# Kernel optimization log

Measured on AMD Instinct MI355X. Metric: run time of the kernel, lower is better.

Reference implementation:

```python
import jax, jax.numpy as jnp
import numpy as np

NUM_GROUPS = 32
EPS = 1e-6


def group_norm(x, gamma, beta):
    # x: [B, C, H, W]; GroupNorm over (channels-in-group, H, W)
    B, C, H, W = x.shape
    xg = x.reshape(B, NUM_GROUPS, C // NUM_GROUPS, H, W)
    mean = xg.mean(axis=(2, 3, 4), keepdims=True)
    var = xg.var(axis=(2, 3, 4), keepdims=True)
    xn = ((xg - mean) * jax.lax.rsqrt(var + EPS)).reshape(B, C, H, W)
    return xn * gamma[None, :, None, None] + beta[None, :, None, None]


def conv1x1(x, w, b):
    # 1x1 conv == channel-mixing matmul. w: [C_out, C_in]
    return jnp.einsum('bchw,oc->bohw', x, w) + b[None, :, None, None]


def setup_inputs() -> dict:
    key = jax.random.key(0)
    ks = jax.random.split(key, 6)
    B, C, H, W = 8, 256, 64, 64
    s = 1.0 / np.sqrt(C)  # fan-in scaled weights (like Conv2d default)
    inp = {
        'x': jax.random.normal(ks[0], (B, C, H, W), jnp.float32),
        'gamma': jnp.ones((C,), jnp.float32),
        'beta': jnp.zeros((C,), jnp.float32),
        'wq': jax.random.normal(ks[1], (C, C), jnp.float32) * s,
        'bq': jnp.zeros((C,), jnp.float32),
        'wk': jax.random.normal(ks[2], (C, C), jnp.float32) * s,
        'bk': jnp.zeros((C,), jnp.float32),
        'wv': jax.random.normal(ks[3], (C, C), jnp.float32) * s,
        'bv': jnp.zeros((C,), jnp.float32),
        'wo': jax.random.normal(ks[4], (C, C), jnp.float32) * s,
        'bo': jnp.zeros((C,), jnp.float32),
    }
    return inp


def reference(x, gamma, beta, wq, bq, wk, bk, wv, bv, wo, bo):
    B, C, H, W = x.shape
    h = group_norm(x, gamma, beta)
    q = conv1x1(h, wq, bq)
    k = conv1x1(h, wk, bk)
    v = conv1x1(h, wv, bv)
    # elu + 1 feature map (nonnegative kernel features)
    q = jax.nn.elu(q) + 1.0
    k = jax.nn.elu(k) + 1.0
    N = H * W
    kf = k.reshape(B, C, N)            # [B, C, N]
    vf = v.reshape(B, C, N)            # [B, C, N]
    qf = q.reshape(B, C, N)            # [B, C, N]
    # kv = k @ v^T : [B, C, C]
    kv = jnp.einsum('bcn,bdn->bcd', kf, vf)
    # h_out[b, n, d] = sum_c q[b, c, n] * kv[b, c, d]; stored channel-first
    h_out = jnp.einsum('bcn,bcd->bdn', qf, kv).reshape(B, C, H, W)
    return x + conv1x1(h_out, wo, bo)
```

## Files before the change

### kernel.cpp

```cpp
#include <hip/hip_runtime.h>
#include <math.h>

#define C_DIM 256
#define N_DIM 4096
#define B_DIM 8

typedef __attribute__((ext_vector_type(8))) short bf16x8;
typedef __attribute__((ext_vector_type(4))) float f32x4;
typedef __attribute__((ext_vector_type(8))) unsigned short us8;
typedef __attribute__((ext_vector_type(4))) unsigned short us4;

__device__ inline unsigned short f2bf(float f) {
    unsigned int u = __float_as_uint(f);
    u += 0x7fffu + ((u >> 16) & 1u);
    return (unsigned short)(u >> 16);
}

__device__ inline void gload_lds16(const void* g, void* l) {
    __builtin_amdgcn_global_load_lds(
        (const __attribute__((address_space(1))) unsigned int*)g,
        (__attribute__((address_space(3))) unsigned int*)l, 16, 0, 0);
}

__global__ __launch_bounds__(256) void prep_kernel(
    const float* __restrict__ wq, const float* __restrict__ wk,
    const float* __restrict__ wv, const float* __restrict__ wo,
    const float* __restrict__ bk, const float* __restrict__ bv,
    const float* __restrict__ x,
    unsigned short* __restrict__ wqb, unsigned short* __restrict__ wkvb,
    unsigned short* __restrict__ wob, float* __restrict__ bkv,
    float2* __restrict__ sums)
{
    int z = blockIdx.x;
    int t = threadIdx.x;
    if (z < 256) {
        const float* s; unsigned short* d;
        int which = z >> 6;
        if (which == 0)      { s = wq; d = wqb; }
        else if (which == 1) { s = wk; d = wkvb; }
        else if (which == 2) { s = wv; d = wkvb + 65536; }
        else                 { s = wo; d = wob; }
        int idx = (z & 63) * 1024 + t * 4;
        float4 v = *(const float4*)(s + idx);
        us4 r; r[0] = f2bf(v.x); r[1] = f2bf(v.y); r[2] = f2bf(v.z); r[3] = f2bf(v.w);
        *(us4*)(d + idx) = r;
    } else if (z == 256) {
        bkv[t]       = bk[t];
        bkv[t + 256] = bv[t];
    } else {
        int bc = z - 257;
        const float* xc = x + (size_t)bc * N_DIM;
        float s = 0.f, q = 0.f;
        for (int i = t; i < 1024; i += 256) {
            float4 v = ((const float4*)xc)[i];
            s += v.x + v.y + v.z + v.w;
            q += v.x*v.x + v.y*v.y + v.z*v.z + v.w*v.w;
        }
        #pragma unroll
        for (int off = 32; off > 0; off >>= 1) {
            s += __shfl_down(s, off);
            q += __shfl_down(q, off);
        }
        __shared__ float red[8];
        int w = t >> 6;
        if ((t & 63) == 0) { red[w*2] = s; red[w*2+1] = q; }
        __syncthreads();
        if (t == 0) {
            sums[bc] = make_float2(red[0]+red[2]+red[4]+red[6],
                                   red[1]+red[3]+red[5]+red[7]);
        }
    }
}

__global__ __launch_bounds__(256) void gn_apply(const float* __restrict__ x,
                                                const float2* __restrict__ sums,
                                                const float* __restrict__ gamma,
                                                const float* __restrict__ beta,
                                                unsigned short* __restrict__ hT) {
    int b = blockIdx.y, n0 = blockIdx.x * 64;
    int t = threadIdx.x;
    __shared__ float scale[256], shift[256];
    __shared__ unsigned short trans[64][264];

    {
        int c = t;
        int gbase = c & ~7;
        float s = 0.f, q = 0.f;
        #pragma unroll
        for (int j = 0; j < 8; j++) {
            float2 u = sums[b*256 + gbase + j];
            s += u.x; q += u.y;
        }
        float mean = s * (1.f/32768.f);
        float var  = q * (1.f/32768.f) - mean*mean;
        float inv  = rsqrtf(var + 1e-6f);
        float gm = gamma[c] * inv;
        scale[c] = gm;
        shift[c] = beta[c] - mean * gm;
    }
    __syncthreads();

    #pragma unroll
    for (int it = 0; it < 16; it++) {
        int c  = it*16 + (t >> 4);
        int nl = (t & 15) * 4;
        float4 v = *(const float4*)(x + ((size_t)(b*C_DIM + c))*N_DIM + n0 + nl);
        float sc = scale[c], sh = shift[c];
        trans[nl+0][c] = f2bf(v.x*sc + sh);
        trans[nl+1][c] = f2bf(v.y*sc + sh);
        trans[nl+2][c] = f2bf(v.z*sc + sh);
        trans[nl+3][c] = f2bf(v.w*sc + sh);
    }
    __syncthreads();

    #pragma unroll
    for (int it = 0; it < 8; it++) {
        int nl = it*8 + (t >> 5);
        int cb = (t & 31) * 8;
        us8 vv = *(us8*)&trans[nl][cb];
        *(us8*)(hT + ((size_t)b*N_DIM + n0 + nl)*C_DIM + cb) = vv;
    }
}

__global__ __launch_bounds__(256) void kvred(const float* __restrict__ src, unsigned short* __restrict__ dst) {
    int gi = (blockIdx.x * 256 + threadIdx.x) * 4;
    int b = gi >> 16, idx = gi & 65535;
    float4 a = make_float4(0.f,0.f,0.f,0.f);
    #pragma unroll
    for (int sp = 0; sp < 8; sp++) {
        float4 v = *(const float4*)(src + (((size_t)b*8 + sp) << 16) + idx);
        a.x += v.x; a.y += v.y; a.z += v.z; a.w += v.w;
    }
    us4 r; r[0] = f2bf(a.x); r[1] = f2bf(a.y); r[2] = f2bf(a.z); r[3] = f2bf(a.w);
    *(us4*)(dst + ((size_t)b << 16) + idx) = r;
}

template<int RI, int RJ, int MODE>
__device__ __forceinline__ void gemm2_body(
    const unsigned short* __restrict__ Ab,
    const unsigned short* __restrict__ Bb,
    const float* __restrict__ bias,
    unsigned short* __restrict__ Cp,
    int crow0, int ccol0, bool elu, char* smem)
{
    constexpr int M = RI * 32, N = RJ * 32;
    constexpr int ACH = M / 64;
    constexpr int BCH = N / 64;
    unsigned short* lds = (unsigned short*)smem;

    int t = threadIdx.x;
    int w = t >> 6, l = t & 63;
    int wm = w >> 1, wn = w & 1;
    int l15 = l & 15, quad = l >> 4;

    f32x4 acc[RI][RJ];
    #pragma unroll
    for (int i = 0; i < RI; i++)
        #pragma unroll
        for (int j = 0; j < RJ; j++)
            #pragma unroll
            for (int r = 0; r < 4; r++) acc[i][j][r] = 0.f;

    auto stage = [&](int buf, int kt) {
        unsigned short* Ls = lds + buf * (M*32 + N*32);
        #pragma unroll
        for (int s = 0; s < ACH; s++) {
            int c = t + s*256, row = c >> 2;
            int cs = (c & 3) ^ ((row >> 1) & 3);
            gload_lds16(Ab + (size_t)row*256 + kt + cs*8, Ls + c*8);
        }
        #pragma unroll
        for (int s = 0; s < BCH; s++) {
            int c = t + s*256, row = c >> 2;
            int cs = (c & 3) ^ ((row >> 1) & 3);
            gload_lds16(Bb + (size_t)row*256 + kt + cs*8, Ls + M*32 + c*8);
        }
    };

    stage(0, 0);
    stage(1, 32);

    int acol = (quad ^ ((l15 >> 1) & 3)) * 8;

    int bufc = 0;
    for (int kt = 0; kt < 8; ++kt) {
        if (kt + 1 < 8) asm volatile("s_waitcnt vmcnt(6)" ::: "memory");
        else            asm volatile("s_waitcnt vmcnt(0)" ::: "memory");
        __builtin_amdgcn_s_barrier();
        __builtin_amdgcn_sched_barrier(0);
        if (kt + 2 < 8) {
            int bufn = bufc + 2; if (bufn >= 3) bufn -= 3;
            stage(bufn, (kt + 2) * 32);
        }
        __builtin_amdgcn_sched_barrier(0);

        const unsigned short* As = lds + bufc * (M*32 + N*32);
        const unsigned short* Bs = As + M*32;
        bf16x8 af[RI], bfr[RJ];
        #pragma unroll
        for (int i = 0; i < RI; i++)
            af[i]  = *(const bf16x8*)(As + (wm*(RI*16) + i*16 + l15)*32 + acol);
        #pragma unroll
        for (int j = 0; j < RJ; j++)
            bfr[j] = *(const bf16x8*)(Bs + (wn*(RJ*16) + j*16 + l15)*32 + acol);
        __builtin_amdgcn_s_setprio(1);
        #pragma unroll
        for (int i = 0; i < RI; i++)
            #pragma unroll
            for (int j = 0; j < RJ; j++)
                acc[i][j] = __builtin_amdgcn_mfma_f32_16x16x32_bf16(af[i], bfr[j], acc[i][j], 0, 0, 0);
        __builtin_amdgcn_s_setprio(0);
        bufc = (bufc == 2) ? 0 : bufc + 1;
    }
    __syncthreads();

    if (MODE == 0) {
        unsigned short* ep = (unsigned short*)smem;
        #pragma unroll
        for (int h = 0; h < 2; h++) {
            if (wm == h) {
                #pragma unroll
                for (int i = 0; i < RI; i++) {
                    #pragma unroll
                    for (int j = 0; j < RJ; j++) {
                        int cl = wn*128 + j*16 + l15;
                        float bi = bias[cl];
                        #pragma unroll
                        for (int r = 0; r < 4; r++) {
                            int rl = quad*4 + i*16 + r;
                            float val = acc[i][j][r] + bi;
                            val = val > 0.f ? val + 1.f : __expf(val);
                            ep[rl*264 + cl] = f2bf(val);
                        }
                    }
                }
            }
            __syncthreads();
            #pragma unroll
            for (int it = 0; it < 8; it++) {
                int row = it*8 + (t >> 5);
                int colc = (t & 31) * 8;
                us8 vv = *(us8*)(ep + row*264 + colc);
                *(us8*)(Cp + (size_t)(crow0 + h*64 + row)*256 + colc) = vv;
            }
            __syncthreads();
        }
    } else {
        unsigned short* ep = (unsigned short*)smem;
        #pragma unroll
        for (int h = 0; h < 2; h++) {
            if (wm == h) {
                #pragma unroll
                for (int i = 0; i < RI; i++) {
                    #pragma unroll
                    for (int j = 0; j < RJ; j++) {
                        int cl = wn*64 + j*16 + l15;
                        #pragma unroll
                        for (int r = 0; r < 4; r++) {
                            int rl = quad*4 + i*16 + r;
                            float val = acc[i][j][r] + bias[crow0 + h*128 + rl];
                            if (elu) val = val > 0.f ? val + 1.f : __expf(val);
                            ep[rl*136 + cl] = f2bf(val);
                        }
                    }
                }
            }
            __syncthreads();
            #pragma unroll
            for (int it = 0; it < 8; it++) {
                int row = it*16 + (t >> 4);
                int colc = (t & 15) * 8;
                us8 vv = *(us8*)(ep + row*136 + colc);
                *(us8*)(Cp + (size_t)(crow0 + h*128 + row)*4096 + ccol0 + colc) = vv;
            }
            __syncthreads();
        }
    }
}

__global__ __launch_bounds__(256, 2) void qkv2(
    const unsigned short* __restrict__ hT, const unsigned short* __restrict__ wqb,
    const unsigned short* __restrict__ wkvb,
    const float* __restrict__ bq, const float* __restrict__ bkv,
    unsigned short* __restrict__ qT, unsigned short* __restrict__ kvbuf)
{
    __shared__ __align__(16) char smem[73728];
    int z = blockIdx.x;
    if (z < 256) {
        int b = z >> 5, m_blk = (z & 31) * 128;
        gemm2_body<4,8,0>(hT + (size_t)b*1048576 + (size_t)m_blk*256, wqb,
                          bq, qT + (size_t)b*1048576, m_blk, 0, true, smem);
    } else {
        int iz = z - 256;
        int b = iz >> 6, rem = iz & 63;
        int mh = rem >> 5, n_blk = (rem & 31) * 128;
        gemm2_body<8,4,1>(wkvb + (size_t)mh*65536,
                          hT + (size_t)b*1048576 + (size_t)n_blk*256,
                          bkv, kvbuf + (size_t)b*2097152,
                          mh*256, n_blk, mh == 0, smem);
    }
}

template<int MODE>
__device__ __forceinline__ void gemm_body(
    const unsigned short* __restrict__ Ab, const unsigned short* __restrict__ Bb,
    const float* __restrict__ bias, const float* __restrict__ residb,
    void* __restrict__ Cb,
    int N, int K, int k0, int Ks, int m_blk, int n_blk, char* smem)
{
    unsigned short* lds = (unsigned short*)smem;

    int t = threadIdx.x;
    int w = t >> 6, l = t & 63;
    int wm = w >> 1, wn = w & 1;
    int l15 = l & 15, quad = l >> 4;

    int srow = w * 16 + (l >> 2);
    int skc  = (((l & 3) ^ ((l >> 3) & 3)) * 8);

    f32x4 acc[4][4];
    #pragma unroll
    for (int i = 0; i < 4; i++)
        #pragma unroll
        for (int j = 0; j < 4; j++)
            #pragma unroll
            for (int r = 0; r < 4; r++) acc[i][j][r] = 0.f;

    auto stage = [&](int buf, int kt) {
        unsigned short* Asl = lds + buf*8192 + t*8;
        unsigned short* Bsl = Asl + 4096;
        #pragma unroll
        for (int rep = 0; rep < 2; rep++) {
            gload_lds16(Ab + (size_t)(m_blk + rep*64 + srow) * K + kt + skc, Asl + rep*2048);
            gload_lds16(Bb + (size_t)(n_blk + rep*64 + srow) * K + kt + skc, Bsl + rep*2048);
        }
    };

    const int nt = Ks >> 5;

    stage(0, k0);
    if (nt > 1) stage(1, k0 + 32);

    int acol = (quad ^ ((l15 >> 1) & 3)) * 8;

    int bufc = 0;
    for (int kt = 0; kt < nt; ++kt) {
        if (kt + 1 < nt) asm volatile("s_waitcnt vmcnt(4)" ::: "memory");
        else             asm volatile("s_waitcnt vmcnt(0)" ::: "memory");
        __builtin_amdgcn_s_barrier();
        __builtin_amdgcn_sched_barrier(0);
        if (kt + 2 < nt) {
            int bufn = bufc + 2; if (bufn >= 3) bufn -= 3;
            stage(bufn, k0 + (kt + 2) * 32);
        }
        __builtin_amdgcn_sched_barrier(0);

        const unsigned short* Aw = lds + bufc*8192 + (wm*64 + l15)*32 + acol;
        const unsigned short* Bw = lds + bufc*8192 + 4096 + (wn*64 + l15)*32 + acol;
        bf16x8 af[4], bfr[4];
        #pragma unroll
        for (int i = 0; i < 4; i++) af[i]  = *(const bf16x8*)(Aw + i*512);
        #pragma unroll
        for (int j = 0; j < 4; j++) bfr[j] = *(const bf16x8*)(Bw + j*512);
        __builtin_amdgcn_s_setprio(1);
        #pragma unroll
        for (int i = 0; i < 4; i++)
            #pragma unroll
            for (int j = 0; j < 4; j++)
                acc[i][j] = __builtin_amdgcn_mfma_f32_16x16x32_bf16(af[i], bfr[j], acc[i][j], 0, 0, 0);
        __builtin_amdgcn_s_setprio(0);
        bufc = (bufc == 2) ? 0 : bufc + 1;
    }
    __syncthreads();

    if (MODE == 4) {
        unsigned short* ep = (unsigned short*)smem;
        unsigned short* Cp = (unsigned short*)Cb;
        #pragma unroll
        for (int h = 0; h < 2; h++) {
            if (wm == h) {
                int row0 = quad*4;
                int col0 = wn*64 + l15;
                #pragma unroll
                for (int i = 0; i < 4; i++)
                    #pragma unroll
                    for (int j = 0; j < 4; j++)
                        #pragma unroll
                        for (int r = 0; r < 4; r++)
                            ep[(row0 + i*16 + r)*136 + col0 + j*16] = f2bf(acc[i][j][r]);
            }
            __syncthreads();
            #pragma unroll
            for (int it = 0; it < 4; it++) {
                int row = it*16 + (t >> 4);
                int col = (t & 15) * 8;
                us8 vv = *(us8*)(ep + row*136 + col);
                *(us8*)(Cp + (size_t)(m_blk + h*64 + row) * N + n_blk + col) = vv;
            }
            __syncthreads();
        }
    } else {
        float* ep32 = (float*)smem;
        float* Cp = (float*)Cb;
        #pragma unroll
        for (int h = 0; h < 2; h++) {
            if (wm == h) {
                int row0 = quad*4;
                int col0 = wn*64 + l15;
                #pragma unroll
                for (int i = 0; i < 4; i++)
                    #pragma unroll
                    for (int j = 0; j < 4; j++)
                        #pragma unroll
                        for (int r = 0; r < 4; r++)
                            ep32[(row0 + i*16 + r)*140 + col0 + j*16] = acc[i][j][r];
            }
            __syncthreads();
            #pragma unroll
            for (int it = 0; it < 8; it++) {
                int rl  = it*8 + (t >> 5);
                int row = m_blk + h*64 + rl;
                int col = (t & 31) * 4;
                f32x4 vv = *(f32x4*)(ep32 + rl*140 + col);
                if (MODE == 5) {
                    float bi = bias[row];
                    float4 rv = *(const float4*)(residb + (size_t)row * N + n_blk + col);
                    vv[0] += bi + rv.x; vv[1] += bi + rv.y;
                    vv[2] += bi + rv.z; vv[3] += bi + rv.w;
                }
                *(f32x4*)(Cp + (size_t)row * N + n_blk + col) = vv;
            }
            __syncthreads();
        }
    }
}

template<int MODE>
__global__ __launch_bounds__(256) void gemm_nt(
    const unsigned short* __restrict__ A, const unsigned short* __restrict__ B,
    const float* __restrict__ bias, const float* __restrict__ resid,
    void* __restrict__ Cout,
    int N, int K, int splits,
    size_t sA, size_t sB, size_t sC, size_t sR, int elem4)
{
    __shared__ __align__(16) char smem[49152];
    int b  = blockIdx.z / splits;
    int sp = blockIdx.z % splits;
    int Ks = K / splits;
    size_t cbase = (MODE == 3) ? ((size_t)(b*splits + sp)) * sC : (size_t)b * sC;
    void* Cb = elem4 ? (void*)((float*)Cout + cbase) : (void*)((unsigned short*)Cout + cbase);
    gemm_body<MODE>(A + b*sA, B + b*sB, bias,
                    resid ? resid + b*sR : nullptr, Cb,
                    N, K, sp*Ks, Ks, blockIdx.y*128, blockIdx.x*128, smem);
}

extern "C" void kernel_launch(void* const* d_in, const int* in_sizes, int n_in,
                              void* d_out, int out_size, void* d_ws, size_t ws_size,
                              hipStream_t stream) {
    const float* x     = (const float*)d_in[0];
    const float* gamma = (const float*)d_in[1];
    const float* beta  = (const float*)d_in[2];
    const float* wq    = (const float*)d_in[3];
    const float* bq    = (const float*)d_in[4];
    const float* wk    = (const float*)d_in[5];
    const float* bk    = (const float*)d_in[6];
    const float* wv    = (const float*)d_in[7];
    const float* bv    = (const float*)d_in[8];
    const float* wo    = (const float*)d_in[9];
    const float* bo    = (const float*)d_in[10];
    float* out = (float*)d_out;

    const size_t TEN = (size_t)B_DIM * C_DIM * N_DIM;
    unsigned short* ws16  = (unsigned short*)d_ws;
    unsigned short* hT    = ws16;
    unsigned short* qT    = hT    + TEN;
    unsigned short* kvbuf = qT    + TEN;
    unsigned short* kvb   = kvbuf + 2*TEN;
    unsigned short* M2b   = kvb   + 524288;
    unsigned short* wqb   = M2b   + 524288;
    unsigned short* wkvb  = wqb   + 65536;
    unsigned short* wob   = wkvb  + 131072;
    float*          bkv   = (float*)(wob + 65536);
    float2*         sums  = (float2*)(bkv + 512);
    float*          kvf   = (float*)(sums + 2048);

    prep_kernel<<<dim3(2305), 256, 0, stream>>>(wq, wk, wv, wo, bk, bv, x,
                                                wqb, wkvb, wob, bkv, sums);
    gn_apply<<<dim3(N_DIM/64, B_DIM), 256, 0, stream>>>(x, sums, gamma, beta, hT);
    qkv2<<<dim3(768), 256, 0, stream>>>(hT, wqb, wkvb, bq, bkv, qT, kvbuf);
    gemm_nt<3><<<dim3(2, 2, B_DIM*8), 256, 0, stream>>>(
        kvbuf, kvbuf + 1048576, nullptr, nullptr, kvf,
        256, 4096, 8, 2097152, 2097152, 65536, 0, 1);
    kvred<<<dim3(512), 256, 0, stream>>>(kvf, kvb);
    gemm_nt<4><<<dim3(2, 2, B_DIM), 256, 0, stream>>>(
        wob, kvb, nullptr, nullptr, M2b,
        256, 256, 1, 0, 65536, 65536, 0, 0);
    gemm_nt<5><<<dim3(32, 2, B_DIM), 256, 0, stream>>>(
        M2b, qT, bo, x, out,
        4096, 256, 1, 65536, 1048576, 1048576, 1048576, 1);
}
```

Baseline: 186.1 us.

## Fuse group-norm apply into QKV projection, keeping normalized tile in LDS

```diff
diff --git a/kernel.cpp b/kernel.cpp
--- a/kernel.cpp
+++ b/kernel.cpp
@@ -72,233 +72,245 @@
     }
 }
 
-__global__ __launch_bounds__(256) void gn_apply(const float* __restrict__ x,
-                                                const float2* __restrict__ sums,
-                                                const float* __restrict__ gamma,
-                                                const float* __restrict__ beta,
-                                                unsigned short* __restrict__ hT) {
-    int b = blockIdx.y, n0 = blockIdx.x * 64;
-    int t = threadIdx.x;
+__global__ __launch_bounds__(256) void kvred(const float* __restrict__ src, unsigned short* __restrict__ dst) {
+    int gi = (blockIdx.x * 256 + threadIdx.x) * 4;
+    int b = gi >> 16, idx = gi & 65535;
+    float4 a = make_float4(0.f,0.f,0.f,0.f);
+    #pragma unroll
+    for (int sp = 0; sp < 8; sp++) {
+        float4 v = *(const float4*)(src + (((size_t)b*8 + sp) << 16) + idx);
+        a.x += v.x; a.y += v.y; a.z += v.z; a.w += v.w;
+    }
+    us4 r; r[0] = f2bf(a.x); r[1] = f2bf(a.y); r[2] = f2bf(a.z); r[3] = f2bf(a.w);
+    *(us4*)(dst + ((size_t)b << 16) + idx) = r;
+}
+
+
+__device__ __forceinline__ void stage_w(const unsigned short* __restrict__ W,
+                                        unsigned short* __restrict__ dst, int kt, int t) {
+    #pragma unroll
+    for (int s = 0; s < 4; s++) {
+        int c = t + s*256;
+        int row = c >> 2, slot = c & 3;
+        int cs = slot ^ ((row >> 1) & 3);
+        gload_lds16(W + (size_t)row*256 + kt + cs*8, dst + c*8);
+    }
+}
+
+__device__ __forceinline__ void phase_kv(
+    const unsigned short* __restrict__ W, const unsigned short* __restrict__ hs,
+    unsigned short* __restrict__ wst, unsigned short* __restrict__ kvdst,
+    const float* __restrict__ biasr, int ccb, int n0, bool elu, int t)
+{
+    int w = t >> 6, l = t & 63;
+    int wm = w >> 1, wn = w & 1;
+    int l15 = l & 15, quad = l >> 4;
+    int acol = (quad ^ ((l15 >> 1) & 3)) * 8;
+    int rsw  = (l15 >> 1) & 3;
+
+    f32x4 acc[8][2];
+    #pragma unroll
+    for (int i = 0; i < 8; i++)
+        #pragma unroll
+        for (int j = 0; j < 2; j++)
+            #pragma unroll
+            for (int r = 0; r < 4; r++) acc[i][j][r] = 0.f;
+
+    stage_w(W, wst, 0, t);
+    asm volatile("s_waitcnt vmcnt(0)" ::: "memory");
+    __syncthreads();
+
+    int buf = 0;
+    for (int kt = 0; kt < 8; ++kt) {
+        if (kt + 1 < 8) stage_w(W, wst + (buf^1)*8192, (kt+1)*32, t);
+        __builtin_amdgcn_sched_barrier(0);
+        bf16x8 af[8], bfr[2];
+        #pragma unroll
+        for (int i = 0; i < 8; i++)
+            af[i] = *(const bf16x8*)(wst + buf*8192 + (wm*128 + i*16 + l15)*32 + acol);
+        #pragma unroll
+        for (int j = 0; j < 2; j++) {
+            int n = wn*32 + j*16 + l15;
+            bfr[j] = *(const bf16x8*)(hs + n*256 + (kt*4 + (quad ^ rsw))*8);
+        }
+        __builtin_amdgcn_s_setprio(1);
+        #pragma unroll
+        for (int i = 0; i < 8; i++)
+            #pragma unroll
+            for (int j = 0; j < 2; j++)
+                acc[i][j] = __builtin_amdgcn_mfma_f32_16x16x32_bf16(af[i], bfr[j], acc[i][j], 0, 0, 0);
+        __builtin_amdgcn_s_setprio(0);
+        __builtin_amdgcn_sched_barrier(0);
+        asm volatile("s_waitcnt vmcnt(0)" ::: "memory");
+        __syncthreads();
+        buf ^= 1;
+    }
+
+    unsigned short* ep = wst;
+    #pragma unroll
+    for (int h = 0; h < 2; h++) {
+        if (wm == h) {
+            #pragma unroll
+            for (int i = 0; i < 8; i++) {
+                #pragma unroll
+                for (int j = 0; j < 2; j++) {
+                    int cl = wn*32 + j*16 + l15;
+                    #pragma unroll
+                    for (int r = 0; r < 4; r++) {
+                        int rloc = i*16 + quad*4 + r;
+                        float val = acc[i][j][r] + biasr[h*128 + rloc];
+                        if (elu) val = val > 0.f ? val + 1.f : __expf(val);
+                        ep[rloc*72 + cl] = f2bf(val);
+                    }
+                }
+            }
+        }
+        __syncthreads();
+        #pragma unroll
+        for (int it = 0; it < 4; it++) {
+            int idx = t + it*256;
+            int row = idx >> 3;
+            int colc = (idx & 7) * 8;
+            us8 vv = *(us8*)(ep + row*72 + colc);
+            *(us8*)(kvdst + (size_t)(ccb + h*128 + row)*4096 + n0 + colc) = vv;
+        }
+        __syncthreads();
+    }
+}
+
+__device__ __forceinline__ void phase_q(
+    const unsigned short* __restrict__ W, const unsigned short* __restrict__ hs,
+    unsigned short* __restrict__ wst, unsigned short* __restrict__ qdst,
+    const float* __restrict__ bq, int n0, int t)
+{
+    int w = t >> 6, l = t & 63;
+    int wm = w >> 1, wn = w & 1;
+    int l15 = l & 15, quad = l >> 4;
+    int acol = (quad ^ ((l15 >> 1) & 3)) * 8;
+    int rsw  = (l15 >> 1) & 3;
+
+    f32x4 acc[2][8];
+    #pragma unroll
+    for (int i = 0; i < 2; i++)
+        #pragma unroll
+        for (int j = 0; j < 8; j++)
+            #pragma unroll
+            for (int r = 0; r < 4; r++) acc[i][j][r] = 0.f;
+
+    stage_w(W, wst, 0, t);
+    asm volatile("s_waitcnt vmcnt(0)" ::: "memory");
+    __syncthreads();
+
+    int buf = 0;
+    for (int kt = 0; kt < 8; ++kt) {
+        if (kt + 1 < 8) stage_w(W, wst + (buf^1)*8192, (kt+1)*32, t);
+        __builtin_amdgcn_sched_barrier(0);
+        bf16x8 af[2], bfr[8];
+        #pragma unroll
+        for (int i = 0; i < 2; i++) {
+            int n = wm*32 + i*16 + l15;
+            af[i] = *(const bf16x8*)(hs + n*256 + (kt*4 + (quad ^ rsw))*8);
+        }
+        #pragma unroll
+        for (int j = 0; j < 8; j++)
+            bfr[j] = *(const bf16x8*)(wst + buf*8192 + (wn*128 + j*16 + l15)*32 + acol);
+        __builtin_amdgcn_s_setprio(1);
+        #pragma unroll
+        for (int i = 0; i < 2; i++)
+            #pragma unroll
+            for (int j = 0; j < 8; j++)
+                acc[i][j] = __builtin_amdgcn_mfma_f32_16x16x32_bf16(af[i], bfr[j], acc[i][j], 0, 0, 0);
+        __builtin_amdgcn_s_setprio(0);
+        __builtin_amdgcn_sched_barrier(0);
+        asm volatile("s_waitcnt vmcnt(0)" ::: "memory");
+        __syncthreads();
+        buf ^= 1;
+    }
+
+    unsigned short* ep = wst;
+    #pragma unroll
+    for (int h = 0; h < 2; h++) {
+        if (wm == h) {
+            #pragma unroll
+            for (int i = 0; i < 2; i++) {
+                #pragma unroll
+                for (int j = 0; j < 8; j++) {
+                    int cl = wn*128 + j*16 + l15;
+                    float bi = bq[cl];
+                    #pragma unroll
+                    for (int r = 0; r < 4; r++) {
+                        int rloc = i*16 + quad*4 + r;
+                        float val = acc[i][j][r] + bi;
+                        val = val > 0.f ? val + 1.f : __expf(val);
+                        ep[rloc*264 + cl] = f2bf(val);
+                    }
+                }
+            }
+        }
+        __syncthreads();
+        #pragma unroll
+        for (int it = 0; it < 4; it++) {
+            int idx = t + it*256;
+            int row = idx >> 5;
+            int colc = (idx & 31) * 8;
+            us8 vv = *(us8*)(ep + row*264 + colc);
+            *(us8*)(qdst + (size_t)(n0 + h*32 + row)*256 + colc) = vv;
+        }
+        __syncthreads();
+    }
+}
+
+__global__ __launch_bounds__(256, 2) void fused_qkv(
+    const float* __restrict__ x, const float2* __restrict__ sums,
+    const float* __restrict__ gamma, const float* __restrict__ beta,
+    const unsigned short* __restrict__ wqb, const unsigned short* __restrict__ wkvb,
+    const float* __restrict__ bq, const float* __restrict__ bkv,
+    unsigned short* __restrict__ qT, unsigned short* __restrict__ kvbuf)
+{
+    __shared__ __align__(16) unsigned short hs[16384];
+    __shared__ __align__(16) unsigned short wst[16384];
     __shared__ float scale[256], shift[256];
-    __shared__ unsigned short trans[64][264];
+
+    int b  = blockIdx.y;
+    int n0 = blockIdx.x * 64;
+    int t  = threadIdx.x;
 
     {
-        int c = t;
-        int gbase = c & ~7;
+        int c = t, gbase = c & ~7;
         float s = 0.f, q = 0.f;
         #pragma unroll
-        for (int j = 0; j < 8; j++) {
-            float2 u = sums[b*256 + gbase + j];
-            s += u.x; q += u.y;
-        }
+        for (int j = 0; j < 8; j++) { float2 u = sums[b*256 + gbase + j]; s += u.x; q += u.y; }
         float mean = s * (1.f/32768.f);
         float var  = q * (1.f/32768.f) - mean*mean;
         float inv  = rsqrtf(var + 1e-6f);
         float gm = gamma[c] * inv;
-        scale[c] = gm;
-        shift[c] = beta[c] - mean * gm;
+        scale[c] = gm; shift[c] = beta[c] - mean*gm;
     }
     __syncthreads();
 
     #pragma unroll
-    for (int it = 0; it < 16; it++) {
-        int c  = it*16 + (t >> 4);
-        int nl = (t & 15) * 4;
-        float4 v = *(const float4*)(x + ((size_t)(b*C_DIM + c))*N_DIM + n0 + nl);
+    for (int it = 0; it < 8; ++it) {
+        int c  = it*32 + (t >> 3);
+        int nl = (t & 7) * 8;
+        const float* xp = x + ((size_t)(b*256 + c))*4096 + n0 + nl;
+        float4 v0 = *(const float4*)xp;
+        float4 v1 = *(const float4*)(xp + 4);
         float sc = scale[c], sh = shift[c];
-        trans[nl+0][c] = f2bf(v.x*sc + sh);
-        trans[nl+1][c] = f2bf(v.y*sc + sh);
-        trans[nl+2][c] = f2bf(v.z*sc + sh);
-        trans[nl+3][c] = f2bf(v.w*sc + sh);
+        int chunk = c >> 3, pos = c & 7;
+        float vv[8] = {v0.x, v0.y, v0.z, v0.w, v1.x, v1.y, v1.z, v1.w};
+        #pragma unroll
+        for (int r = 0; r < 8; ++r) {
+            int n = nl + r;
+            int cs = (chunk & ~3) | ((chunk & 3) ^ ((n >> 1) & 3));
+            hs[n*256 + cs*8 + pos] = f2bf(vv[r] * sc + sh);
+        }
     }
     __syncthreads();
 
-    #pragma unroll
-    for (int it = 0; it < 8; it++) {
-        int nl = it*8 + (t >> 5);
-        int cb = (t & 31) * 8;
-        us8 vv = *(us8*)&trans[nl][cb];
-        *(us8*)(hT + ((size_t)b*N_DIM + n0 + nl)*C_DIM + cb) = vv;
-    }
-}
-
-__global__ __launch_bounds__(256) void kvred(const float* __restrict__ src, unsigned short* __restrict__ dst) {
-    int gi = (blockIdx.x * 256 + threadIdx.x) * 4;
-    int b = gi >> 16, idx = gi & 65535;
-    float4 a = make_float4(0.f,0.f,0.f,0.f);
-    #pragma unroll
-    for (int sp = 0; sp < 8; sp++) {
-        float4 v = *(const float4*)(src + (((size_t)b*8 + sp) << 16) + idx);
-        a.x += v.x; a.y += v.y; a.z += v.z; a.w += v.w;
-    }
-    us4 r; r[0] = f2bf(a.x); r[1] = f2bf(a.y); r[2] = f2bf(a.z); r[3] = f2bf(a.w);
-    *(us4*)(dst + ((size_t)b << 16) + idx) = r;
-}
-
-template<int RI, int RJ, int MODE>
-__device__ __forceinline__ void gemm2_body(
-    const unsigned short* __restrict__ Ab,
-    const unsigned short* __restrict__ Bb,
-    const float* __restrict__ bias,
-    unsigned short* __restrict__ Cp,
-    int crow0, int ccol0, bool elu, char* smem)
-{
-    constexpr int M = RI * 32, N = RJ * 32;
-    constexpr int ACH = M / 64;
-    constexpr int BCH = N / 64;
-    unsigned short* lds = (unsigned short*)smem;
-
-    int t = threadIdx.x;
-    int w = t >> 6, l = t & 63;
-    int wm = w >> 1, wn = w & 1;
-    int l15 = l & 15, quad = l >> 4;
-
-    f32x4 acc[RI][RJ];
-    #pragma unroll
-    for (int i = 0; i < RI; i++)
-        #pragma unroll
-        for (int j = 0; j < RJ; j++)
-            #pragma unroll
-            for (int r = 0; r < 4; r++) acc[i][j][r] = 0.f;
-
-    auto stage = [&](int buf, int kt) {
-        unsigned short* Ls = lds + buf * (M*32 + N*32);
-        #pragma unroll
-        for (int s = 0; s < ACH; s++) {
-            int c = t + s*256, row = c >> 2;
-            int cs = (c & 3) ^ ((row >> 1) & 3);
-            gload_lds16(Ab + (size_t)row*256 + kt + cs*8, Ls + c*8);
-        }
-        #pragma unroll
-        for (int s = 0; s < BCH; s++) {
-            int c = t + s*256, row = c >> 2;
-            int cs = (c & 3) ^ ((row >> 1) & 3);
-            gload_lds16(Bb + (size_t)row*256 + kt + cs*8, Ls + M*32 + c*8);
-        }
-    };
-
-    stage(0, 0);
-    stage(1, 32);
-
-    int acol = (quad ^ ((l15 >> 1) & 3)) * 8;
-
-    int bufc = 0;
-    for (int kt = 0; kt < 8; ++kt) {
-        if (kt + 1 < 8) asm volatile("s_waitcnt vmcnt(6)" ::: "memory");
-        else            asm volatile("s_waitcnt vmcnt(0)" ::: "memory");
-        __builtin_amdgcn_s_barrier();
-        __builtin_amdgcn_sched_barrier(0);
-        if (kt + 2 < 8) {
-            int bufn = bufc + 2; if (bufn >= 3) bufn -= 3;
-            stage(bufn, (kt + 2) * 32);
-        }
-        __builtin_amdgcn_sched_barrier(0);
-
-        const unsigned short* As = lds + bufc * (M*32 + N*32);
-        const unsigned short* Bs = As + M*32;
-        bf16x8 af[RI], bfr[RJ];
-        #pragma unroll
-        for (int i = 0; i < RI; i++)
-            af[i]  = *(const bf16x8*)(As + (wm*(RI*16) + i*16 + l15)*32 + acol);
-        #pragma unroll
-        for (int j = 0; j < RJ; j++)
-            bfr[j] = *(const bf16x8*)(Bs + (wn*(RJ*16) + j*16 + l15)*32 + acol);
-        __builtin_amdgcn_s_setprio(1);
-        #pragma unroll
-        for (int i = 0; i < RI; i++)
-            #pragma unroll
-            for (int j = 0; j < RJ; j++)
-                acc[i][j] = __builtin_amdgcn_mfma_f32_16x16x32_bf16(af[i], bfr[j], acc[i][j], 0, 0, 0);
-        __builtin_amdgcn_s_setprio(0);
-        bufc = (bufc == 2) ? 0 : bufc + 1;
-    }
-    __syncthreads();
-
-    if (MODE == 0) {
-        unsigned short* ep = (unsigned short*)smem;
-        #pragma unroll
-        for (int h = 0; h < 2; h++) {
-            if (wm == h) {
-                #pragma unroll
-                for (int i = 0; i < RI; i++) {
-                    #pragma unroll
-                    for (int j = 0; j < RJ; j++) {
-                        int cl = wn*128 + j*16 + l15;
-                        float bi = bias[cl];
-                        #pragma unroll
-                        for (int r = 0; r < 4; r++) {
-                            int rl = quad*4 + i*16 + r;
-                            float val = acc[i][j][r] + bi;
-                            val = val > 0.f ? val + 1.f : __expf(val);
-                            ep[rl*264 + cl] = f2bf(val);
-                        }
-                    }
-                }
-            }
-            __syncthreads();
-            #pragma unroll
-            for (int it = 0; it < 8; it++) {
-                int row = it*8 + (t >> 5);
-                int colc = (t & 31) * 8;
-                us8 vv = *(us8*)(ep + row*264 + colc);
-                *(us8*)(Cp + (size_t)(crow0 + h*64 + row)*256 + colc) = vv;
-            }
-            __syncthreads();
-        }
-    } else {
-        unsigned short* ep = (unsigned short*)smem;
-        #pragma unroll
-        for (int h = 0; h < 2; h++) {
-            if (wm == h) {
-                #pragma unroll
-                for (int i = 0; i < RI; i++) {
-                    #pragma unroll
-                    for (int j = 0; j < RJ; j++) {
-                        int cl = wn*64 + j*16 + l15;
-                        #pragma unroll
-                        for (int r = 0; r < 4; r++) {
-                            int rl = quad*4 + i*16 + r;
-                            float val = acc[i][j][r] + bias[crow0 + h*128 + rl];
-                            if (elu) val = val > 0.f ? val + 1.f : __expf(val);
-                            ep[rl*136 + cl] = f2bf(val);
-                        }
-                    }
-                }
-            }
-            __syncthreads();
-            #pragma unroll
-            for (int it = 0; it < 8; it++) {
-                int row = it*16 + (t >> 4);
-                int colc = (t & 15) * 8;
-                us8 vv = *(us8*)(ep + row*136 + colc);
-                *(us8*)(Cp + (size_t)(crow0 + h*128 + row)*4096 + ccol0 + colc) = vv;
-            }
-            __syncthreads();
-        }
-    }
-}
-
-__global__ __launch_bounds__(256, 2) void qkv2(
-    const unsigned short* __restrict__ hT, const unsigned short* __restrict__ wqb,
-    const unsigned short* __restrict__ wkvb,
-    const float* __restrict__ bq, const float* __restrict__ bkv,
-    unsigned short* __restrict__ qT, unsigned short* __restrict__ kvbuf)
-{
-    __shared__ __align__(16) char smem[73728];
-    int z = blockIdx.x;
-    if (z < 256) {
-        int b = z >> 5, m_blk = (z & 31) * 128;
-        gemm2_body<4,8,0>(hT + (size_t)b*1048576 + (size_t)m_blk*256, wqb,
-                          bq, qT + (size_t)b*1048576, m_blk, 0, true, smem);
-    } else {
-        int iz = z - 256;
-        int b = iz >> 6, rem = iz & 63;
-        int mh = rem >> 5, n_blk = (rem & 31) * 128;
-        gemm2_body<8,4,1>(wkvb + (size_t)mh*65536,
-                          hT + (size_t)b*1048576 + (size_t)n_blk*256,
-                          bkv, kvbuf + (size_t)b*2097152,
-                          mh*256, n_blk, mh == 0, smem);
-    }
+    unsigned short* kvdst = kvbuf + (size_t)b * 2097152;
+    phase_kv(wkvb,         hs, wst, kvdst, bkv,       0,   n0, true,  t);
+    phase_kv(wkvb + 65536, hs, wst, kvdst, bkv + 256, 256, n0, false, t);
+    phase_q (wqb,          hs, wst, qT + (size_t)b*1048576, bq, n0, t);
 }
 
 template<int MODE>
@@ -486,8 +498,8 @@
 
     prep_kernel<<<dim3(2305), 256, 0, stream>>>(wq, wk, wv, wo, bk, bv, x,
                                                 wqb, wkvb, wob, bkv, sums);
-    gn_apply<<<dim3(N_DIM/64, B_DIM), 256, 0, stream>>>(x, sums, gamma, beta, hT);
-    qkv2<<<dim3(768), 256, 0, stream>>>(hT, wqb, wkvb, bq, bkv, qT, kvbuf);
+    fused_qkv<<<dim3(N_DIM/64, B_DIM), 256, 0, stream>>>(
+        x, sums, gamma, beta, wqb, wkvb, bq, bkv, qT, kvbuf);
     gemm_nt<3><<<dim3(2, 2, B_DIM*8), 256, 0, stream>>>(
         kvbuf, kvbuf + 1048576, nullptr, nullptr, kvf,
         256, 4096, 8, 2097152, 2097152, 65536, 0, 1);
```

Result: faster. 173.9 us (-6.6%).
